# Kernel tuning notes

Hardware: AMD Instinct MI355X
Metric: run time of the kernel (lower is better)

Reference implementation:

```python
import jax, jax.numpy as jnp
import numpy as np

N, IN_DIM, LAT, NB = 4096, 3000, 64, 2
SINKHORN_ITERS = 3


def _bce_logits(x, y):
    # torch BCEWithLogitsLoss, mean reduction, numerically stable
    return jnp.mean(jnp.maximum(x, 0.0) - x * y + jnp.log1p(jnp.exp(-jnp.abs(x))))


def _forward(feature_set, adj_set, graph_neigh_set, label_CSL_set, dist_mat_set,
             enc_W, dec_W, Ms, disc_W, disc_b, perm_idx):
    nb = feature_set.shape[0]
    hs = []
    loss_sl = 0.0
    loss_feat = 0.0
    for k in range(nb):  # small fixed loop over slices
        x, adj, mask, lab = feature_set[k], adj_set[k], graph_neigh_set[k], label_CSL_set[k]
        h = adj @ (x @ enc_W[k])            # GCN encode: spmm(adj, x @ W)
        out = adj @ (h @ dec_W[k])          # GCN decode
        x_a = x[perm_idx[k]]                # permutation(x): row shuffle
        h_a = adj @ (x_a @ enc_W[k])
        hr, har = jax.nn.relu(h), jax.nn.relu(h_a)

        def readout(emb):
            vsum = mask @ emb
            ge = vsum / mask.sum(1, keepdims=True)
            nrm = jnp.linalg.norm(ge, axis=1, keepdims=True)
            return ge / jnp.maximum(nrm, 1e-12)   # F.normalize p=2

        g = jax.nn.sigmoid(readout(hr))
        g_a = jax.nn.sigmoid(readout(har))

        def disc(c, hp, hm):
            s1 = jnp.einsum('nd,de,ne->n', hp, disc_W, c) + disc_b[0]
            s2 = jnp.einsum('nd,de,ne->n', hm, disc_W, c) + disc_b[0]
            return jnp.stack([s1, s2], axis=1)  # [N,2]

        ret = disc(g, hr, har)
        ret_a = disc(g_a, har, hr)
        loss_sl = loss_sl + _bce_logits(ret, lab) + _bce_logits(ret_a, lab)
        loss_feat = loss_feat + jnp.mean((x - out) ** 2)
        hs.append(h)

    loss_align = 0.0; loss_align_fix = 0.0; loss_maintain = 0.0
    loss_marginal = 0.0; loss_sparsity = 0.0
    for k in range(1, nb):
        src, tgt = hs[k - 1], hs[k]
        M = Ms[k - 1]
        m1, m2 = src.shape[0], tgt.shape[0]
        C = (src @ M) @ (tgt @ M).T / jnp.sqrt(jnp.float32(M.shape[0]))
        P = jax.nn.softmax(C, axis=1) / m1
        # NonSquareSinkhornKnopp.fit: alternate row/col normalization to uniform marginals
        for _ in range(SINKHORN_ITERS):
            P = P / (m1 * P.sum(1, keepdims=True))
            P = P / (m2 * P.sum(0, keepdims=True))
        cxy = P / P.sum(1, keepdims=True)
        cyx = P.T / P.T.sum(1, keepdims=True)
        # cdist(src, tgt)
        d2 = jnp.sum(src ** 2, 1)[:, None] + jnp.sum(tgt ** 2, 1)[None, :] - 2.0 * (src @ tgt.T)
        cd = jnp.sqrt(jnp.maximum(d2, 1e-12))
        loss_align = loss_align + jnp.sum(P * cd)
        f0, f1 = feature_set[k - 1], feature_set[k]
        loss_align_fix = loss_align_fix + jnp.mean((f0 - cxy @ f1) ** 2) + jnp.mean((f1 - cyx @ f0) ** 2)
        D0, D1 = dist_mat_set[k - 1], dist_mat_set[k]
        diff1 = D0 - cxy @ (D1 @ cxy.T)
        diff2 = D1 - cyx @ (D0 @ cyx.T)
        loss_maintain = loss_maintain + jnp.linalg.norm(diff1) / m1 + jnp.linalg.norm(diff2) / m2
        # replicate torch F.kl_div(input, target) = mean(target*(log target - input))
        p = jnp.full((m2,), 1.0 / m2, jnp.float32)
        q = P.sum(0)
        kld_pq = jnp.mean(q * (jnp.log(q) - p))
        kld_pp = jnp.mean(p * (jnp.log(p) - p))
        loss_marginal = loss_marginal + (kld_pq - kld_pp) * m2
        loss_sparsity = loss_sparsity - jnp.sum(P * jnp.log(P + 1e-10))
    return jnp.stack([loss_sl, loss_feat, loss_align, loss_align_fix,
                      loss_maintain, loss_marginal, loss_sparsity])


def setup_inputs():
    key = jax.random.key(0)
    ks = jax.random.split(key, 12)
    feature_set = jax.random.normal(ks[0], (NB, N, IN_DIM), jnp.float32)
    A = jax.random.uniform(ks[1], (NB, N, N), jnp.float32)
    adj_set = A / A.sum(-1, keepdims=True)  # row-stochastic dense stand-in for normalized sparse adj
    mask = (jax.random.uniform(ks[2], (NB, N, N)) < 0.01).astype(jnp.float32)
    graph_neigh_set = mask + jnp.eye(N, dtype=jnp.float32)[None]  # nonzero row sums
    lab = jnp.concatenate([jnp.ones((N, 1)), jnp.zeros((N, 1))], axis=1).astype(jnp.float32)
    label_CSL_set = jnp.broadcast_to(lab, (NB, N, 2))
    D = jax.random.uniform(ks[3], (NB, N, N), jnp.float32)
    dist_mat_set = 0.5 * (D + jnp.swapaxes(D, 1, 2))
    perm_idx = jnp.stack([jax.random.permutation(ks[4 + i], N) for i in range(NB)]).astype(jnp.int32)
    s_enc = np.float32(np.sqrt(2.0 / (IN_DIM + LAT)))
    enc_W = jax.random.normal(ks[6], (NB, IN_DIM, LAT), jnp.float32) * s_enc
    dec_W = jax.random.normal(ks[7], (NB, LAT, IN_DIM), jnp.float32) * s_enc
    s_lat = np.float32(np.sqrt(1.0 / LAT))
    Ms = jax.random.normal(ks[8], (NB - 1, LAT, LAT), jnp.float32) * s_lat
    disc_W = jax.random.normal(ks[9], (LAT, LAT), jnp.float32) * s_lat
    disc_b = jnp.zeros((1,), jnp.float32)
    return dict(feature_set=feature_set, adj_set=adj_set, graph_neigh_set=graph_neigh_set,
                label_CSL_set=label_CSL_set, dist_mat_set=dist_mat_set, perm_idx=perm_idx,
                enc_W=enc_W, dec_W=dec_W, Ms=Ms, disc_W=disc_W, disc_b=disc_b)


def reference(feature_set, adj_set, graph_neigh_set, label_CSL_set, dist_mat_set,
              perm_idx, enc_W, dec_W, Ms, disc_W, disc_b):
    return _forward(feature_set, adj_set, graph_neigh_set, label_CSL_set, dist_mat_set,
                    enc_W, dec_W, Ms, disc_W, disc_b, perm_idx)
```

## Files before the change

### kernel.cpp

```cpp
#include <hip/hip_runtime.h>
#include <cmath>

constexpr int kN   = 4096;
constexpr int kIN  = 3000;
constexpr int kINp = 3072;
constexpr int kLAT = 64;

enum { SL = 0, FEAT, ALN, FXA, FXB, SM1, SM2, SPS, NSLOT };

typedef __bf16 bf16x8 __attribute__((ext_vector_type(8)));
typedef float f32x4 __attribute__((ext_vector_type(4)));
typedef unsigned short u16x8 __attribute__((ext_vector_type(8)));
typedef unsigned short u16x4 __attribute__((ext_vector_type(4)));

template<bool IS_MAX>
__device__ __forceinline__ float blk_red(float v) {
  __shared__ float buf[8];
  #pragma unroll
  for (int s = 32; s > 0; s >>= 1) {
    float o = __shfl_down(v, s, 64);
    v = IS_MAX ? fmaxf(v, o) : (v + o);
  }
  int lane = threadIdx.x & 63, wv = threadIdx.x >> 6, nw = blockDim.x >> 6;
  __syncthreads();
  if (lane == 0) buf[wv] = v;
  __syncthreads();
  float r = buf[0];
  for (int i = 1; i < nw; i++) r = IS_MAX ? fmaxf(r, buf[i]) : (r + buf[i]);
  __syncthreads();
  return r;
}

__device__ __forceinline__ float wave_red_sum(float v) {
  #pragma unroll
  for (int s = 32; s > 0; s >>= 1) v += __shfl_down(v, s, 64);
  return v;
}

__device__ __forceinline__ unsigned short f2bf(float f) {
  unsigned u = __builtin_bit_cast(unsigned, f);
  u += 0x7fffu + ((u >> 16) & 1u);
  return (unsigned short)(u >> 16);
}
__device__ __forceinline__ float bf2f(unsigned short h) {
  return __builtin_bit_cast(float, (unsigned)h << 16);
}

__device__ __forceinline__ void gload16(const unsigned short* g, unsigned short* l) {
  __builtin_amdgcn_global_load_lds(
      (const __attribute__((address_space(1))) unsigned int*)g,
      (__attribute__((address_space(3))) unsigned int*)l, 16, 0, 0);
}

#define VMW(n) asm volatile("s_waitcnt vmcnt(" #n ")" ::: "memory")

__device__ __forceinline__ void tri_decode(int lu, int& bx, int& by) {
  int x = lu & 7, i = lu >> 3;
  int u = x * 66 + i;
  float disc = 4225.f - 8.f * (float)u;
  by = (int)((65.f - sqrtf(fmaxf(disc, 0.f))) * 0.5f);
  while (by > 0 && 32 * by - by * (by - 1) / 2 > u) by--;
  while (32 * (by + 1) - (by + 1) * by / 2 <= u) by++;
  bx = by + (u - (32 * by - by * (by - 1) / 2));
}

template<int EPI, int XBF>
__global__ __launch_bounds__(256)
void bt_mfma_k(const unsigned short* __restrict__ A, const unsigned short* __restrict__ Bt,
               unsigned short* __restrict__ Cb, float* __restrict__ Cf,
               const void* __restrict__ Xv,
               const float* __restrict__ rowdiv, const float* __restrict__ coldiv,
               float* __restrict__ slot, int gx, int Nc, int K, int ldX)
{
  __shared__ unsigned short AB[3 * 8192];

  int orig = blockIdx.x;
  int x = orig & 7, tt = orig >> 3;
  int bx = tt >> 2;
  int by = x * 4 + (tt & 3);
  const int row0 = by * 128, col0 = bx * 128;

  const int t = threadIdx.x, l = t & 63, wv = t >> 6;
  const int wr = wv >> 1, wc = wv & 1;
  const int lr = l & 15, lkh = (l >> 4) << 3;

  f32x4 acc[4][4];
  #pragma unroll
  for (int i = 0; i < 4; i++)
    #pragma unroll
    for (int j = 0; j < 4; j++) acc[i][j] = (f32x4){0.f, 0.f, 0.f, 0.f};

  const int srow = l >> 2;
  const int sk   = (l & 3) << 3;
  const unsigned short* Ab = A  + (size_t)(row0 + srow) * K + sk;
  const unsigned short* Bb = Bt + (size_t)(col0 + srow) * K + sk;

  const int NT = K >> 5;

  auto STAGE = [&](int kt, int buf) {
    unsigned short* As = AB + buf * 8192;
    unsigned short* Bs = As + 4096;
    int k0 = kt << 5;
    #pragma unroll
    for (int h2 = 0; h2 < 2; h2++) {
      int c = wv * 2 + h2;
      gload16(Ab + (size_t)c * 16 * K + k0, As + c * 512);
      gload16(Bb + (size_t)c * 16 * K + k0, Bs + c * 512);
    }
  };

  STAGE(0, 0);
  if (NT > 1) STAGE(1, 1);
  if (NT > 2) STAGE(2, 2);
  int cur = 0;

  for (int kt = 0; kt < NT; ++kt) {
    int ahead = NT - 1 - kt;
    if (ahead >= 2)      { VMW(8); }
    else if (ahead == 1) { VMW(4); }
    else                 { VMW(0); }
    __builtin_amdgcn_sched_barrier(0);
    __builtin_amdgcn_s_barrier();

    const unsigned short* As = AB + cur * 8192;
    const unsigned short* Bs = As + 4096;
    u16x8 af[4], bfv[4];
    #pragma unroll
    for (int mi = 0; mi < 4; mi++)
      af[mi] = *(const u16x8*)&As[(wr * 64 + mi * 16 + lr) * 32 + lkh];
    #pragma unroll
    for (int ni = 0; ni < 4; ni++)
      bfv[ni] = *(const u16x8*)&Bs[(wc * 64 + ni * 16 + lr) * 32 + lkh];
    #pragma unroll
    for (int mi = 0; mi < 4; mi++)
      #pragma unroll
      for (int ni = 0; ni < 4; ni++)
        acc[mi][ni] = __builtin_amdgcn_mfma_f32_16x16x32_bf16(
            __builtin_bit_cast(bf16x8, af[mi]),
            __builtin_bit_cast(bf16x8, bfv[ni]), acc[mi][ni], 0, 0, 0);

    __builtin_amdgcn_s_barrier();
    if (kt + 3 < NT) STAGE(kt + 3, cur);
    cur = (cur == 2) ? 0 : cur + 1;
  }

  const int lcol = l & 15, lrow = (l >> 4) << 2;
  if (EPI == 0) {
    #pragma unroll
    for (int mi = 0; mi < 4; mi++) {
      int rr = row0 + wr * 64 + mi * 16 + lrow;
      #pragma unroll
      for (int ni = 0; ni < 4; ni++) {
        int cc = col0 + wc * 64 + ni * 16 + lcol;
        #pragma unroll
        for (int r = 0; r < 4; r++) {
          float v = acc[mi][ni][r];
          if (rowdiv) v /= rowdiv[rr + r];
          Cb[(size_t)(rr + r) * 4096 + cc] = f2bf(v);
        }
      }
    }
  } else if (EPI == 1) {
    #pragma unroll
    for (int mi = 0; mi < 4; mi++) {
      int rr = row0 + wr * 64 + mi * 16 + lrow;
      #pragma unroll
      for (int ni = 0; ni < 4; ni++) {
        int cc = col0 + wc * 64 + ni * 16 + lcol;
        #pragma unroll
        for (int r = 0; r < 4; r++)
          Cf[(size_t)(rr + r) * 4096 + cc] = acc[mi][ni][r];
      }
    }
  } else if (EPI == 2) {
    const float* Xf = (const float*)Xv;
    const unsigned short* Xh = (const unsigned short*)Xv;
    float part = 0.f;
    #pragma unroll
    for (int mi = 0; mi < 4; mi++) {
      int rr = row0 + wr * 64 + mi * 16 + lrow;
      #pragma unroll
      for (int ni = 0; ni < 4; ni++) {
        int cc = col0 + wc * 64 + ni * 16 + lcol;
        if (cc < Nc) {
          float cd = coldiv ? coldiv[cc] : 1.f;
          #pragma unroll
          for (int r = 0; r < 4; r++) {
            float v = acc[mi][ni][r];
            if (rowdiv) v /= rowdiv[rr + r];
            v /= cd;
            size_t xi = (size_t)(rr + r) * ldX + cc;
            float xval = XBF ? bf2f(Xh[xi]) : Xf[xi];
            float d = xval - v;
            part = fmaf(d, d, part);
          }
        }
      }
    }
    part = blk_red<false>(part);
    if (t == 0) atomicAdd(slot, part);
  } else {
    const unsigned short* Ph = (const unsigned short*)Xv;
    float a = 0.f, sp = 0.f;
    #pragma unroll
    for (int mi = 0; mi < 4; mi++) {
      int rr = row0 + wr * 64 + mi * 16 + lrow;
      #pragma unroll
      for (int ni = 0; ni < 4; ni++) {
        int cc = col0 + wc * 64 + ni * 16 + lcol;
        #pragma unroll
        for (int r = 0; r < 4; r++) {
          float g = acc[mi][ni][r];
          float p = bf2f(Ph[(size_t)(rr + r) * ldX + cc]);
          float d2 = rowdiv[rr + r] + coldiv[cc] - 2.f * g;
          a = fmaf(p, sqrtf(fmaxf(d2, 1e-12f)), a);
          sp = fmaf(p, logf(p + 1e-10f), sp);
        }
      }
    }
    a = blk_red<false>(a);
    sp = blk_red<false>(sp);
    if (t == 0) { atomicAdd(&slot[ALN], a); atomicAdd(&slot[SPS], sp); }
  }
}

template<int XBF, int SYM>
__global__ __launch_bounds__(256)
void bt2_mfma_k(const unsigned short* __restrict__ A0, const unsigned short* __restrict__ B0,
                const void* __restrict__ X0, const float* __restrict__ rd0,
                const float* __restrict__ cd0, float* __restrict__ slot0,
                const unsigned short* __restrict__ A1, const unsigned short* __restrict__ B1,
                const void* __restrict__ X1, const float* __restrict__ rd1,
                const float* __restrict__ cd1, float* __restrict__ slot1,
                int gx, int Nc, int K, int ldX, int ntiles, int split)
{
  __shared__ unsigned short AB[3 * 8192];
  const int t = threadIdx.x, l = t & 63, wv = t >> 6;
  const int wr = wv >> 1, wc = wv & 1;
  const int lr = l & 15, lkh = (l >> 4) << 3;
  const int srow = l >> 2;
  const int sk   = (l & 3) << 3;
  const int NT = K >> 5;

  for (int u = blockIdx.x; u < ntiles; u += gridDim.x) {
    const int s1 = (u >= split);
    const int lu = s1 ? (u - split) : u;
    const unsigned short* A  = s1 ? A1 : A0;
    const unsigned short* Bt = s1 ? B1 : B0;
    const void* Xv           = s1 ? X1 : X0;
    const float* rowdiv      = s1 ? rd1 : rd0;
    const float* coldiv      = s1 ? cd1 : cd0;
    float* slot              = s1 ? slot1 : slot0;

    int bx, by;
    if (SYM) {
      tri_decode(lu, bx, by);
    } else {
      int x = lu & 7, tt = lu >> 3;
      bx = tt >> 2;
      by = x * 4 + (tt & 3);
    }
    const int row0 = by * 128, col0 = bx * 128;

    f32x4 acc[4][4];
    #pragma unroll
    for (int i = 0; i < 4; i++)
      #pragma unroll
      for (int j = 0; j < 4; j++) acc[i][j] = (f32x4){0.f, 0.f, 0.f, 0.f};

    const unsigned short* Ab = A  + (size_t)(row0 + srow) * K + sk;
    const unsigned short* Bb = Bt + (size_t)(col0 + srow) * K + sk;

    auto STAGE = [&](int kt, int buf) {
      unsigned short* As = AB + buf * 8192;
      unsigned short* Bs = As + 4096;
      int k0 = kt << 5;
      #pragma unroll
      for (int h2 = 0; h2 < 2; h2++) {
        int c = wv * 2 + h2;
        gload16(Ab + (size_t)c * 16 * K + k0, As + c * 512);
        gload16(Bb + (size_t)c * 16 * K + k0, Bs + c * 512);
      }
    };

    STAGE(0, 0);
    if (NT > 1) STAGE(1, 1);
    if (NT > 2) STAGE(2, 2);
    int cur = 0;

    for (int kt = 0; kt < NT; ++kt) {
      int ahead = NT - 1 - kt;
      if (ahead >= 2)      { VMW(8); }
      else if (ahead == 1) { VMW(4); }
      else                 { VMW(0); }
      __builtin_amdgcn_sched_barrier(0);
      __builtin_amdgcn_s_barrier();

      const unsigned short* As = AB + cur * 8192;
      const unsigned short* Bs = As + 4096;
      u16x8 af[4], bfv[4];
      #pragma unroll
      for (int mi = 0; mi < 4; mi++)
        af[mi] = *(const u16x8*)&As[(wr * 64 + mi * 16 + lr) * 32 + lkh];
      #pragma unroll
      for (int ni = 0; ni < 4; ni++)
        bfv[ni] = *(const u16x8*)&Bs[(wc * 64 + ni * 16 + lr) * 32 + lkh];
      #pragma unroll
      for (int mi = 0; mi < 4; mi++)
        #pragma unroll
        for (int ni = 0; ni < 4; ni++)
          acc[mi][ni] = __builtin_amdgcn_mfma_f32_16x16x32_bf16(
              __builtin_bit_cast(bf16x8, af[mi]),
              __builtin_bit_cast(bf16x8, bfv[ni]), acc[mi][ni], 0, 0, 0);

      __builtin_amdgcn_s_barrier();
      if (kt + 3 < NT) STAGE(kt + 3, cur);
      cur = (cur == 2) ? 0 : cur + 1;
    }

    const int lcol = l & 15, lrow = (l >> 4) << 2;
    const float* Xf = (const float*)Xv;
    const unsigned short* Xh = (const unsigned short*)Xv;
    float part = 0.f;
    #pragma unroll
    for (int mi = 0; mi < 4; mi++) {
      int rr = row0 + wr * 64 + mi * 16 + lrow;
      #pragma unroll
      for (int ni = 0; ni < 4; ni++) {
        int cc = col0 + wc * 64 + ni * 16 + lcol;
        if (cc < Nc) {
          float cd = coldiv ? coldiv[cc] : 1.f;
          #pragma unroll
          for (int r = 0; r < 4; r++) {
            float v = acc[mi][ni][r];
            if (rowdiv) v /= rowdiv[rr + r];
            v /= cd;
            size_t xi = (size_t)(rr + r) * ldX + cc;
            float xval = XBF ? bf2f(Xh[xi]) : Xf[xi];
            float d = xval - v;
            part = fmaf(d, d, part);
          }
        }
      }
    }
    part = blk_red<false>(part);
    if (t == 0) {
      float wgt = (SYM && col0 > row0) ? 2.f : 1.f;
      atomicAdd(slot, part * wgt);
    }
    __syncthreads();
  }
}

__global__ __launch_bounds__(256)
void ns_mfma_k(const unsigned short* __restrict__ A, const unsigned short* __restrict__ Bt,
               float* __restrict__ C, int Nc, int K, int KC, int ldC)
{
  __shared__ unsigned short AB[2 * 8192];
  int ks = blockIdx.x & 15, strip = blockIdx.x >> 4;
  const int row0 = strip * 128;
  const int kbase = ks * KC;

  const int t = threadIdx.x, l = t & 63, wv = t >> 6;
  const int wr = wv >> 1, wc = wv & 1;
  const int lr = l & 15, lkh = (l >> 4) << 3;

  f32x4 acc[4][4];
  #pragma unroll
  for (int i = 0; i < 4; i++)
    #pragma unroll
    for (int j = 0; j < 4; j++) acc[i][j] = (f32x4){0.f, 0.f, 0.f, 0.f};

  const int srow = l >> 2;
  const int sk   = (l & 3) << 3;
  const unsigned short* Ab = A  + (size_t)(row0 + srow) * K + kbase + sk;
  const unsigned short* Bb = Bt + (size_t)srow * K + kbase + sk;

  const int NT = KC >> 5;

  auto STAGE = [&](int kt, int buf) {
    unsigned short* As = AB + buf * 8192;
    unsigned short* Bs = As + 4096;
    int k0 = kt << 5;
    #pragma unroll
    for (int h2 = 0; h2 < 2; h2++) {
      int c = wv * 2 + h2;
      gload16(Ab + (size_t)c * 16 * K + k0, As + c * 512);
      gload16(Bb + (size_t)c * 16 * K + k0, Bs + c * 512);
    }
  };

  STAGE(0, 0);
  if (NT > 1) STAGE(1, 1);
  int cur = 0;

  for (int kt = 0; kt < NT; ++kt) {
    if (kt + 1 < NT) { VMW(4); }
    else             { VMW(0); }
    __builtin_amdgcn_sched_barrier(0);
    __builtin_amdgcn_s_barrier();

    const unsigned short* As = AB + cur * 8192;
    const unsigned short* Bs = As + 4096;
    u16x8 af[4], bfv[4];
    #pragma unroll
    for (int mi = 0; mi < 4; mi++)
      af[mi] = *(const u16x8*)&As[(wr * 64 + mi * 16 + lr) * 32 + lkh];
    #pragma unroll
    for (int ni = 0; ni < 4; ni++)
      bfv[ni] = *(const u16x8*)&Bs[(wc * 64 + ni * 16 + lr) * 32 + lkh];
    #pragma unroll
    for (int mi = 0; mi < 4; mi++)
      #pragma unroll
      for (int ni = 0; ni < 4; ni++)
        acc[mi][ni] = __builtin_amdgcn_mfma_f32_16x16x32_bf16(
            __builtin_bit_cast(bf16x8, af[mi]),
            __builtin_bit_cast(bf16x8, bfv[ni]), acc[mi][ni], 0, 0, 0);

    __builtin_amdgcn_s_barrier();
    if (kt + 2 < NT) STAGE(kt + 2, cur);
    cur ^= 1;
  }

  const int lcol = l & 15, lrow = (l >> 4) << 2;
  #pragma unroll
  for (int mi = 0; mi < 4; mi++) {
    int rr = row0 + wr * 64 + mi * 16 + lrow;
    #pragma unroll
    for (int ni = 0; ni < 4; ni++) {
      int cc = wc * 64 + ni * 16 + lcol;
      if (cc < Nc) {
        #pragma unroll
        for (int r = 0; r < 4; r++)
          atomicAdd(&C[(size_t)(rr + r) * ldC + cc], acc[mi][ni][r]);
      }
    }
  }
}

__global__ void cvt_k(const float* __restrict__ s, unsigned short* __restrict__ d,
                      int n8, float scale)
{
  int i = blockIdx.x * 256 + threadIdx.x;
  if (i < n8) {
    float4 a = ((const float4*)s)[2 * i], b = ((const float4*)s)[2 * i + 1];
    u16x8 w;
    w[0] = f2bf(a.x * scale); w[1] = f2bf(a.y * scale);
    w[2] = f2bf(a.z * scale); w[3] = f2bf(a.w * scale);
    w[4] = f2bf(b.x * scale); w[5] = f2bf(b.y * scale);
    w[6] = f2bf(b.z * scale); w[7] = f2bf(b.w * scale);
    ((u16x8*)d)[i] = w;
  }
}

__global__ void cvt_rs_k(const float* __restrict__ s, unsigned short* __restrict__ d,
                         float* __restrict__ mrs)
{
  int i = blockIdx.x * 256 + threadIdx.x;
  float4 a = ((const float4*)s)[2 * i], b = ((const float4*)s)[2 * i + 1];
  u16x8 w;
  w[0] = f2bf(a.x); w[1] = f2bf(a.y); w[2] = f2bf(a.z); w[3] = f2bf(a.w);
  w[4] = f2bf(b.x); w[5] = f2bf(b.y); w[6] = f2bf(b.z); w[7] = f2bf(b.w);
  ((u16x8*)d)[i] = w;
  float s8 = a.x + a.y + a.z + a.w + b.x + b.y + b.z + b.w;
  float ws = wave_red_sum(s8);
  if ((threadIdx.x & 63) == 0) atomicAdd(&mrs[i >> 9], ws);
}

__global__ void cvt_pad_k(const float* __restrict__ s, unsigned short* __restrict__ d)
{
  int i = blockIdx.x * 256 + threadIdx.x;
  int row = i / 384, c8 = (i - row * 384) * 8;
  u16x8 w = (u16x8)0;
  if (c8 < kIN) {
    const float* sp = s + (size_t)row * kIN + c8;
    float4 a = *(const float4*)sp, b = *(const float4*)(sp + 4);
    w[0] = f2bf(a.x); w[1] = f2bf(a.y); w[2] = f2bf(a.z); w[3] = f2bf(a.w);
    w[4] = f2bf(b.x); w[5] = f2bf(b.y); w[6] = f2bf(b.z); w[7] = f2bf(b.w);
  }
  ((u16x8*)d)[i] = w;
}

__global__ void cvtsq_k(const float* __restrict__ H, unsigned short* __restrict__ hb,
                        float* __restrict__ outv)
{
  int row = blockIdx.x * 4 + (threadIdx.x >> 6), j = threadIdx.x & 63;
  float v = H[(size_t)row * 128 + j];
  hb[(size_t)row * 64 + j] = f2bf(v);
  float p = wave_red_sum(v * v);
  if (j == 0) outv[row] = p;
}

template<bool RELU>
__global__ void tr_k(const float* __restrict__ src, unsigned short* __restrict__ dst,
                     int R, int C, int sld, int dld)
{
  __shared__ float tile[32][33];
  int c0 = blockIdx.x * 32, r0 = blockIdx.y * 32;
  int tr_ = threadIdx.x >> 3, tc4 = (threadIdx.x & 7) << 2;
  #pragma unroll
  for (int j = 0; j < 4; j++) {
    int r = r0 + tr_, c = c0 + tc4 + j;
    float v = (r < R && c < C) ? src[(size_t)r * sld + c] : 0.f;
    if (RELU) v = fmaxf(v, 0.f);
    tile[tr_][tc4 + j] = v;
  }
  __syncthreads();
  u16x4 wv;
  #pragma unroll
  for (int j = 0; j < 4; j++) wv[j] = f2bf(tile[tc4 + j][tr_]);
  *(u16x4*)&dst[(size_t)(c0 + tr_) * dld + r0 + tc4] = wv;
}

__global__ void tr_bf_k(const unsigned short* __restrict__ src,
                        unsigned short* __restrict__ dst, int R, int C)
{
  __shared__ unsigned short tile[32][36];
  int c0 = blockIdx.x * 32, r0 = blockIdx.y * 32;
  int tr_ = threadIdx.x >> 3, tc4 = (threadIdx.x & 7) << 2;
  *(u16x4*)&tile[tr_][tc4] = *(const u16x4*)&src[(size_t)(r0 + tr_) * C + c0 + tc4];
  __syncthreads();
  u16x4 w;
  #pragma unroll
  for (int j = 0; j < 4; j++) w[j] = tile[tc4 + j][tr_];
  *(u16x4*)&dst[(size_t)(c0 + tr_) * R + r0 + tc4] = w;
}

template<bool RELU>
__global__ __launch_bounds__(256)
void gemm_small_k(const float* __restrict__ A, const float* __restrict__ B,
                  float* __restrict__ C, int M, int Nc, int K,
                  int ldA, int ldB, int ldC)
{
  __shared__ float As[16][68];
  __shared__ float Bs[16][68];
  int tid = threadIdx.x;
  int tx = tid & 15, ty = tid >> 4;
  int row0 = blockIdx.y * 64, col0 = blockIdx.x * 64;
  float acc[4][4] = {};

  for (int k0 = 0; k0 < K; k0 += 16) {
    {
      int m = tid >> 2, kk = (tid & 3) << 2;
      const float* ap = A + (size_t)(row0 + m) * ldA + k0 + kk;
      float4 v = *(const float4*)ap;
      if (RELU) {
        v.x = fmaxf(v.x, 0.f); v.y = fmaxf(v.y, 0.f);
        v.z = fmaxf(v.z, 0.f); v.w = fmaxf(v.w, 0.f);
      }
      As[kk + 0][m] = v.x; As[kk + 1][m] = v.y; As[kk + 2][m] = v.z; As[kk + 3][m] = v.w;
    }
    {
      int kk = tid >> 4, c = (tid & 15) << 2;
      const float* bp = B + (size_t)(k0 + kk) * ldB + col0 + c;
      #pragma unroll
      for (int i = 0; i < 4; i++)
        Bs[kk][c + i] = (col0 + c + i < Nc) ? bp[i] : 0.f;
    }
    __syncthreads();
    #pragma unroll
    for (int kk = 0; kk < 16; kk++) {
      float4 a4 = *(const float4*)&As[kk][ty << 2];
      float4 b4 = *(const float4*)&Bs[kk][tx << 2];
      float av[4] = {a4.x, a4.y, a4.z, a4.w};
      float bv[4] = {b4.x, b4.y, b4.z, b4.w};
      #pragma unroll
      for (int i = 0; i < 4; i++)
        #pragma unroll
        for (int j = 0; j < 4; j++)
          acc[i][j] = fmaf(av[i], bv[j], acc[i][j]);
    }
    __syncthreads();
  }
  #pragma unroll
  for (int i = 0; i < 4; i++) {
    int r = row0 + (ty << 2) + i;
    #pragma unroll
    for (int j = 0; j < 4; j++) {
      int c = col0 + (tx << 2) + j;
      if (c < Nc) C[(size_t)r * ldC + c] = acc[i][j];
    }
  }
}

__global__ __launch_bounds__(256)
void sink_k(float* __restrict__ P, unsigned short* __restrict__ Pb,
            const float* __restrict__ cs_in, float* __restrict__ cs_out,
            float* __restrict__ rs, int mode)
{
  int tid = threadIdx.x;
  int r0 = blockIdx.x * 8;
  float csl[16] = {};
  float cdiv[16];
  if (mode != 0) {
    #pragma unroll
    for (int t = 0; t < 4; t++) {
      float4 c4 = ((const float4*)cs_in)[tid + t * 256];
      cdiv[4 * t + 0] = 1.f / (4096.f * c4.x);
      cdiv[4 * t + 1] = 1.f / (4096.f * c4.y);
      cdiv[4 * t + 2] = 1.f / (4096.f * c4.z);
      cdiv[4 * t + 3] = 1.f / (4096.f * c4.w);
    }
  }
  for (int rr = 0; rr < 8; rr++) {
    int row = r0 + rr;
    float4* prow = (float4*)(P + (size_t)row * 4096);
    float4 r[4];
    #pragma unroll
    for (int t = 0; t < 4; t++) r[t] = prow[tid + t * 256];

    if (mode == 0) {
      float m = -3.4e38f;
      #pragma unroll
      for (int t = 0; t < 4; t++)
        m = fmaxf(m, fmaxf(fmaxf(r[t].x, r[t].y), fmaxf(r[t].z, r[t].w)));
      m = blk_red<true>(m);
      float s = 0.f;
      #pragma unroll
      for (int t = 0; t < 4; t++) {
        r[t].x = expf(r[t].x - m); r[t].y = expf(r[t].y - m);
        r[t].z = expf(r[t].z - m); r[t].w = expf(r[t].w - m);
        s += r[t].x + r[t].y + r[t].z + r[t].w;
      }
      s = blk_red<false>(s);
      float f = 1.f / (s * 4096.f);
      #pragma unroll
      for (int t = 0; t < 4; t++) {
        r[t].x *= f; r[t].y *= f; r[t].z *= f; r[t].w *= f;
        prow[tid + t * 256] = r[t];
        csl[4 * t + 0] += r[t].x; csl[4 * t + 1] += r[t].y;
        csl[4 * t + 2] += r[t].z; csl[4 * t + 3] += r[t].w;
      }
    } else {
      float s = 0.f;
      #pragma unroll
      for (int t = 0; t < 4; t++) {
        r[t].x *= cdiv[4 * t + 0]; r[t].y *= cdiv[4 * t + 1];
        r[t].z *= cdiv[4 * t + 2]; r[t].w *= cdiv[4 * t + 3];
        s += r[t].x + r[t].y + r[t].z + r[t].w;
      }
      s = blk_red<false>(s);
      if (mode == 1) {
        float f = 1.f / (4096.f * s);
        #pragma unroll
        for (int t = 0; t < 4; t++) {
          r[t].x *= f; r[t].y *= f; r[t].z *= f; r[t].w *= f;
          prow[tid + t * 256] = r[t];
          csl[4 * t + 0] += r[t].x; csl[4 * t + 1] += r[t].y;
          csl[4 * t + 2] += r[t].z; csl[4 * t + 3] += r[t].w;
        }
      } else {
        if (tid == 0) rs[row] = s;
        #pragma unroll
        for (int t = 0; t < 4; t++) {
          prow[tid + t * 256] = r[t];
          u16x4 w;
          w[0] = f2bf(r[t].x); w[1] = f2bf(r[t].y);
          w[2] = f2bf(r[t].z); w[3] = f2bf(r[t].w);
          *(u16x4*)&Pb[(size_t)row * 4096 + 4 * (tid + t * 256)] = w;
          csl[4 * t + 0] += r[t].x; csl[4 * t + 1] += r[t].y;
          csl[4 * t + 2] += r[t].z; csl[4 * t + 3] += r[t].w;
        }
      }
    }
  }
  #pragma unroll
  for (int t = 0; t < 4; t++) {
    int j = 4 * (tid + t * 256);
    atomicAdd(&cs_out[j + 0], csl[4 * t + 0]);
    atomicAdd(&cs_out[j + 1], csl[4 * t + 1]);
    atomicAdd(&cs_out[j + 2], csl[4 * t + 2]);
    atomicAdd(&cs_out[j + 3], csl[4 * t + 3]);
  }
}

__global__ void gather_k(float* __restrict__ XP, const int* __restrict__ perm)
{
  int gid = blockIdx.x * 256 + threadIdx.x;
  int i = gid >> 6, j = gid & 63;
  XP[(size_t)i * 128 + 64 + j] = XP[(size_t)perm[i] * 128 + j];
}

__global__ void readout_k(const float* __restrict__ vs2, const float* __restrict__ mrs,
                          float* __restrict__ g2)
{
  int q = blockIdx.x, j = threadIdx.x;
  float v = vs2[(size_t)q * 64 + j] / mrs[q >> 1];
  float p = v * v;
  #pragma unroll
  for (int s = 1; s < 64; s <<= 1) p += __shfl_xor(p, s, 64);
  float nrm = sqrtf(p);
  v = v / fmaxf(nrm, 1e-12f);
  g2[(size_t)q * 64 + j] = 1.f / (1.f + expf(-v));
}

__device__ __forceinline__ float bce_term(float x, float y) {
  return fmaxf(x, 0.f) - x * y + log1pf(expf(-fabsf(x)));
}

__global__ void disc_k(const float* __restrict__ G2, const float* __restrict__ W2,
                       const float* __restrict__ lab, const float* __restrict__ bptr,
                       float* __restrict__ acc)
{
  int i = blockIdx.x, j = threadIdx.x;
  float gj  = G2[(size_t)(2 * i) * 64 + j];
  float gaj = G2[(size_t)(2 * i + 1) * 64 + j];
  float hw  = W2[(size_t)(2 * i) * 64 + j];
  float haw = W2[(size_t)(2 * i + 1) * 64 + j];
  float s1 = hw * gj, s2 = haw * gj, s1a = haw * gaj, s2a = hw * gaj;
  #pragma unroll
  for (int s = 1; s < 64; s <<= 1) {
    s1  += __shfl_xor(s1, s, 64);
    s2  += __shfl_xor(s2, s, 64);
    s1a += __shfl_xor(s1a, s, 64);
    s2a += __shfl_xor(s2a, s, 64);
  }
  if (j == 0) {
    float b = bptr[0];
    float y0 = lab[i * 2 + 0], y1 = lab[i * 2 + 1];
    float t = bce_term(s1 + b, y0) + bce_term(s2 + b, y1)
            + bce_term(s1a + b, y0) + bce_term(s2a + b, y1);
    atomicAdd(&acc[SL], t);
  }
}

__global__ __launch_bounds__(256)
void finalize_k(const float* __restrict__ acc, const float* __restrict__ cs,
                float* __restrict__ out)
{
  int tid = threadIdx.x;
  float invm2 = 1.f / (float)kN;
  float t = 0.f;
  for (int j = tid; j < kN; j += 256) {
    float q = cs[j];
    t += q * (logf(q) - invm2);
  }
  t = blk_red<false>(t);
  if (tid == 0) {
    float kld_pq = t * invm2;
    float kld_pp = invm2 * (logf(invm2) - invm2);
    out[0] = acc[SL] / (2.f * (float)kN);
    out[1] = acc[FEAT] / ((float)kN * (float)kIN);
    out[2] = acc[ALN];
    out[3] = (acc[FXA] + acc[FXB]) / ((float)kN * (float)kIN);
    out[4] = sqrtf(acc[SM1]) / (float)kN + sqrtf(acc[SM2]) / (float)kN;
    out[5] = (kld_pq - kld_pp) * (float)kN;
    out[6] = -acc[SPS];
  }
}

extern "C" void kernel_launch(void* const* d_in, const int* in_sizes, int n_in,
                              void* d_out, int out_size, void* d_ws, size_t ws_size,
                              hipStream_t stream)
{
  (void)in_sizes; (void)n_in; (void)out_size; (void)ws_size;
  const float* feat  = (const float*)d_in[0];
  const float* adjs  = (const float*)d_in[1];
  const float* gmask = (const float*)d_in[2];
  const float* labs  = (const float*)d_in[3];
  const float* dists = (const float*)d_in[4];
  const int*   perms = (const int*)d_in[5];
  const float* encW  = (const float*)d_in[6];
  const float* decW  = (const float*)d_in[7];
  const float* MsW   = (const float*)d_in[8];
  const float* discW = (const float*)d_in[9];
  const float* discb = (const float*)d_in[10];
  float* out = (float*)d_out;

  const size_t SZNN = (size_t)kN * kN;

  char* cur = (char*)d_ws;
  auto alloc = [&](size_t bytes) {
    char* p = cur;
    cur += (bytes + 255) & ~(size_t)255;
    return p;
  };
  float* P            = (float*)alloc(SZNN * 4);
  unsigned short* Pb  = (unsigned short*)alloc(SZNN * 2);
  unsigned short* PbT = (unsigned short*)alloc(SZNN * 2);
  unsigned short* Db  = (unsigned short*)alloc(SZNN * 2);
  unsigned short* ajb = (unsigned short*)alloc(SZNN * 2);
  unsigned short* xb0 = (unsigned short*)alloc((size_t)kN * kINp * 2);
  unsigned short* xb1 = (unsigned short*)alloc((size_t)kN * kINp * 2);
  unsigned short* dWtb= (unsigned short*)alloc((size_t)kINp * kLAT * 2);
  unsigned short* ahb = (unsigned short*)alloc((size_t)kN * kLAT * 2);
  unsigned short* encWtp = (unsigned short*)alloc((size_t)128 * kINp * 2);
  unsigned short* XPt = (unsigned short*)alloc((size_t)128 * kN * 2);
  unsigned short* hbTp= (unsigned short*)alloc((size_t)128 * kN * 2);
  unsigned short* HRt = (unsigned short*)alloc((size_t)128 * kN * 2);
  unsigned short* smb = (unsigned short*)alloc((size_t)kN * kLAT * 2);
  unsigned short* tmb = (unsigned short*)alloc((size_t)kN * kLAT * 2);
  unsigned short* h0b = (unsigned short*)alloc((size_t)kN * kLAT * 2);
  unsigned short* h1b = (unsigned short*)alloc((size_t)kN * kLAT * 2);
  float* XP  = (float*)alloc((size_t)kN * 128 * 4);
  float* HH0 = (float*)alloc((size_t)kN * 128 * 4);
  float* HH1 = (float*)alloc((size_t)kN * 128 * 4);
  float* VS  = (float*)alloc((size_t)kN * 128 * 4);
  float* G2  = (float*)alloc((size_t)kN * 128 * 4);
  float* W2  = (float*)alloc((size_t)kN * 128 * 4);
  float* SM_ = (float*)alloc((size_t)kN * kLAT * 4);
  float* TM_ = (float*)alloc((size_t)kN * kLAT * 4);
  float* ah  = (float*)alloc((size_t)kN * kLAT * 4);
  float* sns = (float*)alloc(kN * 4);
  float* snt = (float*)alloc(kN * 4);
  float* rs  = (float*)alloc(kN * 4);
  float* cs  = (float*)alloc(kN * 4);
  float* csA = (float*)alloc(kN * 4);
  float* csB = (float*)alloc(kN * 4);
  float* mrs = (float*)alloc(kN * 4);
  float* acc = (float*)alloc(NSLOT * 4);

  unsigned short* Tb1 = (unsigned short*)P;
  unsigned short* ftb = ajb;
  unsigned short* ftb2= Db;
  unsigned short* Tb2 = ajb;

  hipMemsetAsync(acc, 0, NSLOT * sizeof(float), stream);

  for (int k = 0; k < 2; k++) {
    const float* x    = feat  + (size_t)k * kN * kIN;
    const float* adj  = adjs  + (size_t)k * SZNN;
    const float* msk  = gmask + (size_t)k * SZNN;
    const float* lab  = labs  + (size_t)k * kN * 2;
    const int*   perm = perms + (size_t)k * kN;
    const float* eW   = encW  + (size_t)k * kIN * kLAT;
    const float* dW   = decW  + (size_t)k * kLAT * kIN;
    float* HHk = (k == 0) ? HH0 : HH1;
    unsigned short* xbk = (k == 0) ? xb0 : xb1;

    cvt_pad_k<<<6144, 256, 0, stream>>>(x, xbk);
    hipMemsetAsync(encWtp, 0, (size_t)128 * kINp * 2, stream);
    tr_k<false><<<dim3(2, (kIN + 31) / 32), 256, 0, stream>>>(eW, encWtp, kIN, kLAT, kLAT, kINp);
    hipMemsetAsync(XP, 0, (size_t)kN * 128 * 4, stream);
    ns_mfma_k<<<512, 256, 0, stream>>>(xbk, encWtp, XP, kLAT, kINp, kINp / 16, 128);
    gather_k<<<kN * 64 / 256, 256, 0, stream>>>(XP, perm);
    tr_k<false><<<dim3(4, 128), 256, 0, stream>>>(XP, XPt, kN, 128, 128, kN);
    cvt_k<<<(int)(SZNN / 8 / 256), 256, 0, stream>>>(adj, ajb, (int)(SZNN / 8), 1.f);
    hipMemsetAsync(HHk, 0, (size_t)kN * 128 * 4, stream);
    ns_mfma_k<<<512, 256, 0, stream>>>(ajb, XPt, HHk, 128, kN, kN / 16, 128);
    hipMemsetAsync(hbTp, 0, (size_t)128 * kN * 2, stream);
    tr_k<false><<<dim3(2, 128), 256, 0, stream>>>(HHk, hbTp, kN, kLAT, 128, kN);
    hipMemsetAsync(ah, 0, (size_t)kN * kLAT * 4, stream);
    ns_mfma_k<<<512, 256, 0, stream>>>(ajb, hbTp, ah, kLAT, kN, kN / 16, kLAT);
    cvt_k<<<128, 256, 0, stream>>>(ah, ahb, kN * kLAT / 8, 1.f);
    tr_k<false><<<dim3(kINp / 32, 2), 256, 0, stream>>>(dW, dWtb, kLAT, kIN, kIN, kLAT);
    bt_mfma_k<2, 1><<<(kINp / 128) * 32, 256, 0, stream>>>(
        ahb, dWtb, nullptr, nullptr, xbk, nullptr, nullptr, &acc[FEAT],
        kINp / 128, kIN, kLAT, kINp);
    tr_k<true><<<dim3(4, 128), 256, 0, stream>>>(HHk, HRt, kN, 128, 128, kN);
    hipMemsetAsync(mrs, 0, kN * 4, stream);
    cvt_rs_k<<<(int)(SZNN / 8 / 256), 256, 0, stream>>>(msk, ajb, mrs);
    hipMemsetAsync(VS, 0, (size_t)kN * 128 * 4, stream);
    ns_mfma_k<<<512, 256, 0, stream>>>(ajb, HRt, VS, 128, kN, kN / 16, 128);
    readout_k<<<2 * kN, 64, 0, stream>>>(VS, mrs, G2);
    gemm_small_k<true><<<dim3(1, 128), 256, 0, stream>>>(HHk, discW, W2, 2 * kN, kLAT,
                                                         kLAT, kLAT, kLAT, kLAT);
    disc_k<<<kN, 64, 0, stream>>>(G2, W2, lab, discb, acc);
  }

  const float* D0 = dists;
  const float* D1 = dists + SZNN;

  gemm_small_k<false><<<dim3(1, 64), 256, 0, stream>>>(HH0, MsW, SM_, kN, kLAT, kLAT,
                                                       128, kLAT, kLAT);
  gemm_small_k<false><<<dim3(1, 64), 256, 0, stream>>>(HH1, MsW, TM_, kN, kLAT, kLAT,
                                                       128, kLAT, kLAT);
  cvt_k<<<128, 256, 0, stream>>>(SM_, smb, kN * kLAT / 8, 0.125f);
  cvt_k<<<128, 256, 0, stream>>>(TM_, tmb, kN * kLAT / 8, 1.f);
  bt_mfma_k<1, 0><<<1024, 256, 0, stream>>>(smb, tmb, nullptr, P, nullptr, nullptr, nullptr,
                                            nullptr, 32, kN, kLAT, 0);

  hipMemsetAsync(csA, 0, kN * 4, stream);
  sink_k<<<512, 256, 0, stream>>>(P, nullptr, nullptr, csA, nullptr, 0);
  hipMemsetAsync(csB, 0, kN * 4, stream);
  sink_k<<<512, 256, 0, stream>>>(P, nullptr, csA, csB, nullptr, 1);
  hipMemsetAsync(csA, 0, kN * 4, stream);
  sink_k<<<512, 256, 0, stream>>>(P, nullptr, csB, csA, nullptr, 1);
  hipMemsetAsync(cs, 0, kN * 4, stream);
  sink_k<<<512, 256, 0, stream>>>(P, Pb, csA, cs, rs, 2);

  tr_k<false><<<dim3(kN / 32, kN / 32), 256, 0, stream>>>(P, PbT, kN, kN, kN, kN);

  cvtsq_k<<<1024, 256, 0, stream>>>(HH0, h0b, sns);
  cvtsq_k<<<1024, 256, 0, stream>>>(HH1, h1b, snt);
  bt_mfma_k<3, 1><<<1024, 256, 0, stream>>>(h0b, h1b, nullptr, nullptr, Pb, sns, snt, acc,
                                            32, kN, kLAT, kN);

  tr_bf_k<<<dim3(kINp / 32, kN / 32), 256, 0, stream>>>(xb1, ftb, kN, kINp);
  tr_bf_k<<<dim3(kINp / 32, kN / 32), 256, 0, stream>>>(xb0, ftb2, kN, kINp);
  bt2_mfma_k<1, 0><<<1024, 256, 0, stream>>>(
      Pb,  ftb,  xb0, rs, nullptr, &acc[FXA],
      PbT, ftb2, xb1, cs, nullptr, &acc[FXB],
      kINp / 128, kIN, kN, kINp, 2 * (kINp / 128) * 32, (kINp / 128) * 32);

  cvt_k<<<(int)(SZNN / 8 / 256), 256, 0, stream>>>(D1, Db, (int)(SZNN / 8), 1.f);
  bt_mfma_k<0, 0><<<1024, 256, 0, stream>>>(Pb, Db, Tb1, nullptr, nullptr, rs, nullptr,
                                            nullptr, 32, kN, kN, 0);
  cvt_k<<<(int)(SZNN / 8 / 256), 256, 0, stream>>>(D0, Db, (int)(SZNN / 8), 1.f);
  bt_mfma_k<0, 0><<<1024, 256, 0, stream>>>(PbT, Db, Tb2, nullptr, nullptr, cs, nullptr,
                                            nullptr, 32, kN, kN, 0);
  bt2_mfma_k<0, 1><<<1024, 256, 0, stream>>>(
      Tb1, Pb,  D0, nullptr, rs, &acc[SM1],
      Tb2, PbT, D1, nullptr, cs, &acc[SM2],
      32, kN, kN, kN, 1056, 528);

  finalize_k<<<1, 256, 0, stream>>>(acc, cs, out);
}
```

Before: 2.132 ms.

## Split fused symmetric structure GEMMs into per-side launches reusing one temp buffer

The combined persistent bt2 kernel that evaluated both structure-matching symmetric GEMMs is replaced by two separate bt_mfma_k launches (EPI 2 with triangular tile decoding and an off-diagonal weight of 2). These are interleaved with the T-producing GEMMs so a single temporary buffer is reused and T stays hot in cache between producer and consumer. The feature-transport GEMM becomes a non-persistent one-tile-per-block kernel specialised for bf16 X and row division. This adds launches and serialises the two sides, trading fewer passes over cold memory for less concurrency within each kernel.

After: 1.987 ms. -6.8%, faster.

```diff
diff --git a/kernel.cpp b/kernel.cpp
--- a/kernel.cpp
+++ b/kernel.cpp
@@ -70,14 +70,19 @@
                unsigned short* __restrict__ Cb, float* __restrict__ Cf,
                const void* __restrict__ Xv,
                const float* __restrict__ rowdiv, const float* __restrict__ coldiv,
-               float* __restrict__ slot, int gx, int Nc, int K, int ldX)
+               float* __restrict__ slot, int gx, int Nc, int K, int ldX, int sym)
 {
   __shared__ unsigned short AB[3 * 8192];
 
   int orig = blockIdx.x;
-  int x = orig & 7, tt = orig >> 3;
-  int bx = tt >> 2;
-  int by = x * 4 + (tt & 3);
+  int bx, by;
+  if (EPI == 2 && sym) {
+    tri_decode(orig, bx, by);
+  } else {
+    int x = orig & 7, tt = orig >> 3;
+    bx = tt >> 2;
+    by = x * 4 + (tt & 3);
+  }
   const int row0 = by * 128, col0 = bx * 128;
 
   const int t = threadIdx.x, l = t & 63, wv = t >> 6;
@@ -198,7 +203,10 @@
       }
     }
     part = blk_red<false>(part);
-    if (t == 0) atomicAdd(slot, part);
+    if (t == 0) {
+      float wgt = (sym && col0 > row0) ? 2.f : 1.f;
+      atomicAdd(slot, part * wgt);
+    }
   } else {
     const unsigned short* Ph = (const unsigned short*)Xv;
     float a = 0.f, sp = 0.f;
@@ -224,132 +232,115 @@
   }
 }
 
-template<int XBF, int SYM>
 __global__ __launch_bounds__(256)
-void bt2_mfma_k(const unsigned short* __restrict__ A0, const unsigned short* __restrict__ B0,
-                const void* __restrict__ X0, const float* __restrict__ rd0,
-                const float* __restrict__ cd0, float* __restrict__ slot0,
-                const unsigned short* __restrict__ A1, const unsigned short* __restrict__ B1,
-                const void* __restrict__ X1, const float* __restrict__ rd1,
-                const float* __restrict__ cd1, float* __restrict__ slot1,
-                int gx, int Nc, int K, int ldX, int ntiles, int split)
+void bt2f_mfma_k(const unsigned short* __restrict__ A0, const unsigned short* __restrict__ B0,
+                 const unsigned short* __restrict__ X0, const float* __restrict__ rd0,
+                 float* __restrict__ slot0,
+                 const unsigned short* __restrict__ A1, const unsigned short* __restrict__ B1,
+                 const unsigned short* __restrict__ X1, const float* __restrict__ rd1,
+                 float* __restrict__ slot1,
+                 int gx, int Nc, int K, int ldX, int split)
 {
   __shared__ unsigned short AB[3 * 8192];
+
+  int u = blockIdx.x;
+  const int s1 = (u >= split);
+  const int lu = s1 ? (u - split) : u;
+  const unsigned short* A  = s1 ? A1 : A0;
+  const unsigned short* Bt = s1 ? B1 : B0;
+  const unsigned short* Xh = s1 ? X1 : X0;
+  const float* rowdiv      = s1 ? rd1 : rd0;
+  float* slot              = s1 ? slot1 : slot0;
+
+  int x = lu & 7, tt = lu >> 3;
+  int bx = tt >> 2;
+  int by = x * 4 + (tt & 3);
+  const int row0 = by * 128, col0 = bx * 128;
+
   const int t = threadIdx.x, l = t & 63, wv = t >> 6;
   const int wr = wv >> 1, wc = wv & 1;
   const int lr = l & 15, lkh = (l >> 4) << 3;
+
+  f32x4 acc[4][4];
+  #pragma unroll
+  for (int i = 0; i < 4; i++)
+    #pragma unroll
+    for (int j = 0; j < 4; j++) acc[i][j] = (f32x4){0.f, 0.f, 0.f, 0.f};
+
   const int srow = l >> 2;
   const int sk   = (l & 3) << 3;
+  const unsigned short* Ab = A  + (size_t)(row0 + srow) * K + sk;
+  const unsigned short* Bb = Bt + (size_t)(col0 + srow) * K + sk;
+
   const int NT = K >> 5;
 
-  for (int u = blockIdx.x; u < ntiles; u += gridDim.x) {
-    const int s1 = (u >= split);
-    const int lu = s1 ? (u - split) : u;
-    const unsigned short* A  = s1 ? A1 : A0;
-    const unsigned short* Bt = s1 ? B1 : B0;
-    const void* Xv           = s1 ? X1 : X0;
-    const float* rowdiv      = s1 ? rd1 : rd0;
-    const float* coldiv      = s1 ? cd1 : cd0;
-    float* slot              = s1 ? slot1 : slot0;
-
-    int bx, by;
-    if (SYM) {
-      tri_decode(lu, bx, by);
-    } else {
-      int x = lu & 7, tt = lu >> 3;
-      bx = tt >> 2;
-      by = x * 4 + (tt & 3);
-    }
-    const int row0 = by * 128, col0 = bx * 128;
-
-    f32x4 acc[4][4];
-    #pragma unroll
-    for (int i = 0; i < 4; i++)
-      #pragma unroll
-      for (int j = 0; j < 4; j++) acc[i][j] = (f32x4){0.f, 0.f, 0.f, 0.f};
-
-    const unsigned short* Ab = A  + (size_t)(row0 + srow) * K + sk;
-    const unsigned short* Bb = Bt + (size_t)(col0 + srow) * K + sk;
-
-    auto STAGE = [&](int kt, int buf) {
-      unsigned short* As = AB + buf * 8192;
-      unsigned short* Bs = As + 4096;
-      int k0 = kt << 5;
-      #pragma unroll
-      for (int h2 = 0; h2 < 2; h2++) {
-        int c = wv * 2 + h2;
-        gload16(Ab + (size_t)c * 16 * K + k0, As + c * 512);
-        gload16(Bb + (size_t)c * 16 * K + k0, Bs + c * 512);
-      }
-    };
-
-    STAGE(0, 0);
-    if (NT > 1) STAGE(1, 1);
-    if (NT > 2) STAGE(2, 2);
-    int cur = 0;
-
-    for (int kt = 0; kt < NT; ++kt) {
-      int ahead = NT - 1 - kt;
-      if (ahead >= 2)      { VMW(8); }
-      else if (ahead == 1) { VMW(4); }
-      else                 { VMW(0); }
-      __builtin_amdgcn_sched_barrier(0);
-      __builtin_amdgcn_s_barrier();
-
-      const unsigned short* As = AB + cur * 8192;
-      const unsigned short* Bs = As + 4096;
-      u16x8 af[4], bfv[4];
-      #pragma unroll
-      for (int mi = 0; mi < 4; mi++)
-        af[mi] = *(const u16x8*)&As[(wr * 64 + mi * 16 + lr) * 32 + lkh];
+  auto STAGE = [&](int kt, int buf) {
+    unsigned short* As = AB + buf * 8192;
+    unsigned short* Bs = As + 4096;
+    int k0 = kt << 5;
+    #pragma unroll
+    for (int h2 = 0; h2 < 2; h2++) {
+      int c = wv * 2 + h2;
+      gload16(Ab + (size_t)c * 16 * K + k0, As + c * 512);
+      gload16(Bb + (size_t)c * 16 * K + k0, Bs + c * 512);
+    }
+  };
+
+  STAGE(0, 0);
+  if (NT > 1) STAGE(1, 1);
+  if (NT > 2) STAGE(2, 2);
+  int cur = 0;
+
+  for (int kt = 0; kt < NT; ++kt) {
+    int ahead = NT - 1 - kt;
+    if (ahead >= 2)      { VMW(8); }
+    else if (ahead == 1) { VMW(4); }
+    else                 { VMW(0); }
+    __builtin_amdgcn_sched_barrier(0);
+    __builtin_amdgcn_s_barrier();
+
+    const unsigned short* As = AB + cur * 8192;
+    const unsigned short* Bs = As + 4096;
+    u16x8 af[4], bfv[4];
+    #pragma unroll
+    for (int mi = 0; mi < 4; mi++)
+      af[mi] = *(const u16x8*)&As[(wr * 64 + mi * 16 + lr) * 32 + lkh];
+    #pragma unroll
+    for (int ni = 0; ni < 4; ni++)
+      bfv[ni] = *(const u16x8*)&Bs[(wc * 64 + ni * 16 + lr) * 32 + lkh];
+    #pragma unroll
+    for (int mi = 0; mi < 4; mi++)
       #pragma unroll
       for (int ni = 0; ni < 4; ni++)
-        bfv[ni] = *(const u16x8*)&Bs[(wc * 64 + ni * 16 + lr) * 32 + lkh];
-      #pragma unroll
-      for (int mi = 0; mi < 4; mi++)
+        acc[mi][ni] = __builtin_amdgcn_mfma_f32_16x16x32_bf16(
+            __builtin_bit_cast(bf16x8, af[mi]),
+            __builtin_bit_cast(bf16x8, bfv[ni]), acc[mi][ni], 0, 0, 0);
+
+    __builtin_amdgcn_s_barrier();
+    if (kt + 3 < NT) STAGE(kt + 3, cur);
+    cur = (cur == 2) ? 0 : cur + 1;
+  }
+
+  const int lcol = l & 15, lrow = (l >> 4) << 2;
+  float part = 0.f;
+  #pragma unroll
+  for (int mi = 0; mi < 4; mi++) {
+    int rr = row0 + wr * 64 + mi * 16 + lrow;
+    #pragma unroll
+    for (int ni = 0; ni < 4; ni++) {
+      int cc = col0 + wc * 64 + ni * 16 + lcol;
+      if (cc < Nc) {
         #pragma unroll
-        for (int ni = 0; ni < 4; ni++)
-          acc[mi][ni] = __builtin_amdgcn_mfma_f32_16x16x32_bf16(
-              __builtin_bit_cast(bf16x8, af[mi]),
-              __builtin_bit_cast(bf16x8, bfv[ni]), acc[mi][ni], 0, 0, 0);
-
-      __builtin_amdgcn_s_barrier();
-      if (kt + 3 < NT) STAGE(kt + 3, cur);
-      cur = (cur == 2) ? 0 : cur + 1;
-    }
-
-    const int lcol = l & 15, lrow = (l >> 4) << 2;
-    const float* Xf = (const float*)Xv;
-    const unsigned short* Xh = (const unsigned short*)Xv;
-    float part = 0.f;
-    #pragma unroll
-    for (int mi = 0; mi < 4; mi++) {
-      int rr = row0 + wr * 64 + mi * 16 + lrow;
-      #pragma unroll
-      for (int ni = 0; ni < 4; ni++) {
-        int cc = col0 + wc * 64 + ni * 16 + lcol;
-        if (cc < Nc) {
-          float cd = coldiv ? coldiv[cc] : 1.f;
-          #pragma unroll
-          for (int r = 0; r < 4; r++) {
-            float v = acc[mi][ni][r];
-            if (rowdiv) v /= rowdiv[rr + r];
-            v /= cd;
-            size_t xi = (size_t)(rr + r) * ldX + cc;
-            float xval = XBF ? bf2f(Xh[xi]) : Xf[xi];
-            float d = xval - v;
-            part = fmaf(d, d, part);
-          }
+        for (int r = 0; r < 4; r++) {
+          float v = acc[mi][ni][r] / rowdiv[rr + r];
+          float d = bf2f(Xh[(size_t)(rr + r) * ldX + cc]) - v;
+          part = fmaf(d, d, part);
         }
       }
     }
-    part = blk_red<false>(part);
-    if (t == 0) {
-      float wgt = (SYM && col0 > row0) ? 2.f : 1.f;
-      atomicAdd(slot, part * wgt);
-    }
-    __syncthreads();
-  }
+  }
+  part = blk_red<false>(part);
+  if (t == 0) atomicAdd(slot, part);
 }
 
 __global__ __launch_bounds__(256)
@@ -810,10 +801,9 @@
   float* mrs = (float*)alloc(kN * 4);
   float* acc = (float*)alloc(NSLOT * 4);
 
-  unsigned short* Tb1 = (unsigned short*)P;
+  unsigned short* Tb  = (unsigned short*)P;
   unsigned short* ftb = ajb;
   unsigned short* ftb2= Db;
-  unsigned short* Tb2 = ajb;
 
   hipMemsetAsync(acc, 0, NSLOT * sizeof(float), stream);
 
@@ -846,7 +836,7 @@
     tr_k<false><<<dim3(kINp / 32, 2), 256, 0, stream>>>(dW, dWtb, kLAT, kIN, kIN, kLAT);
     bt_mfma_k<2, 1><<<(kINp / 128) * 32, 256, 0, stream>>>(
         ahb, dWtb, nullptr, nullptr, xbk, nullptr, nullptr, &acc[FEAT],
-        kINp / 128, kIN, kLAT, kINp);
+        kINp / 128, kIN, kLAT, kINp, 0);
     tr_k<true><<<dim3(4, 128), 256, 0, stream>>>(HHk, HRt, kN, 128, 128, kN);
     hipMemsetAsync(mrs, 0, kN * 4, stream);
     cvt_rs_k<<<(int)(SZNN / 8 / 256), 256, 0, stream>>>(msk, ajb, mrs);
@@ -868,7 +858,7 @@
   cvt_k<<<128, 256, 0, stream>>>(SM_, smb, kN * kLAT / 8, 0.125f);
   cvt_k<<<128, 256, 0, stream>>>(TM_, tmb, kN * kLAT / 8, 1.f);
   bt_mfma_k<1, 0><<<1024, 256, 0, stream>>>(smb, tmb, nullptr, P, nullptr, nullptr, nullptr,
-                                            nullptr, 32, kN, kLAT, 0);
+                                            nullptr, 32, kN, kLAT, 0, 0);
 
   hipMemsetAsync(csA, 0, kN * 4, stream);
   sink_k<<<512, 256, 0, stream>>>(P, nullptr, nullptr, csA, nullptr, 0);
@@ -884,25 +874,25 @@
   cvtsq_k<<<1024, 256, 0, stream>>>(HH0, h0b, sns);
   cvtsq_k<<<1024, 256, 0, stream>>>(HH1, h1b, snt);
   bt_mfma_k<3, 1><<<1024, 256, 0, stream>>>(h0b, h1b, nullptr, nullptr, Pb, sns, snt, acc,
-                                            32, kN, kLAT, kN);
+                                            32, kN, kLAT, kN, 0);
 
   tr_bf_k<<<dim3(kINp / 32, kN / 32), 256, 0, stream>>>(xb1, ftb, kN, kINp);
   tr_bf_k<<<dim3(kINp / 32, kN / 32), 256, 0, stream>>>(xb0, ftb2, kN, kINp);
-  bt2_mfma_k<1, 0><<<1024, 256, 0, stream>>>(
-      Pb,  ftb,  xb0, rs, nullptr, &acc[FXA],
-      PbT, ftb2, xb1, cs, nullptr, &acc[FXB],
-      kINp / 128, kIN, kN, kINp, 2 * (kINp / 128) * 32, (kINp / 128) * 32);
+  bt2f_mfma_k<<<2 * (kINp / 128) * 32, 256, 0, stream>>>(
+      Pb,  ftb,  xb0, rs, &acc[FXA],
+      PbT, ftb2, xb1, cs, &acc[FXB],
+      kINp / 128, kIN, kN, kINp, (kINp / 128) * 32);
 
   cvt_k<<<(int)(SZNN / 8 / 256), 256, 0, stream>>>(D1, Db, (int)(SZNN / 8), 1.f);
-  bt_mfma_k<0, 0><<<1024, 256, 0, stream>>>(Pb, Db, Tb1, nullptr, nullptr, rs, nullptr,
-                                            nullptr, 32, kN, kN, 0);
+  bt_mfma_k<0, 0><<<1024, 256, 0, stream>>>(Pb, Db, Tb, nullptr, nullptr, rs, nullptr,
+                                            nullptr, 32, kN, kN, 0, 0);
+  bt_mfma_k<2, 0><<<528, 256, 0, stream>>>(Tb, Pb, nullptr, nullptr, D0, nullptr, rs,
+                                           &acc[SM1], 32, kN, kN, kN, 1);
   cvt_k<<<(int)(SZNN / 8 / 256), 256, 0, stream>>>(D0, Db, (int)(SZNN / 8), 1.f);
-  bt_mfma_k<0, 0><<<1024, 256, 0, stream>>>(PbT, Db, Tb2, nullptr, nullptr, cs, nullptr,
-                                            nullptr, 32, kN, kN, 0);
-  bt2_mfma_k<0, 1><<<1024, 256, 0, stream>>>(
-      Tb1, Pb,  D0, nullptr, rs, &acc[SM1],
-      Tb2, PbT, D1, nullptr, cs, &acc[SM2],
-      32, kN, kN, kN, 1056, 528);
+  bt_mfma_k<0, 0><<<1024, 256, 0, stream>>>(PbT, Db, Tb, nullptr, nullptr, cs, nullptr,
+                                            nullptr, 32, kN, kN, 0, 0);
+  bt_mfma_k<2, 0><<<528, 256, 0, stream>>>(Tb, PbT, nullptr, nullptr, D1, nullptr, cs,
+                                           &acc[SM2], 32, kN, kN, kN, 1);
 
   finalize_k<<<1, 256, 0, stream>>>(acc, cs, out);
 }
```
